# Performance work log

Hardware: AMD Instinct MI355X
Metric: run time of the kernel (lower is better)

Reference implementation:

```python
import jax, jax.numpy as jnp
import numpy as np

B, IN, H = 16384, 1024, 1024


def setup_inputs() -> dict:
    key = jax.random.key(0)
    ks = jax.random.split(key, 16)
    stdv = 1.0 / np.sqrt(H)
    u = lambda k, shape: jax.random.uniform(k, shape, jnp.float32, -stdv, stdv)
    return {
        "input": jax.random.normal(ks[0], (B, IN), jnp.float32),
        "prev_h": jax.random.normal(ks[1], (B, H), jnp.float32),
        "prev_c": jax.random.normal(ks[2], (B, H), jnp.float32),
        "weight_xi": u(ks[3], (IN, H)), "weight_hi": u(ks[4], (H, H)),
        "weight_xf": u(ks[5], (IN, H)), "weight_hf": u(ks[6], (H, H)),
        "weight_xu": u(ks[7], (IN, H)), "weight_hu": u(ks[8], (H, H)),
        "weight_xo": u(ks[9], (IN, H)), "weight_ho": u(ks[10], (H, H)),
        "bias_i": u(ks[11], (H,)), "bias_f": u(ks[12], (H,)),
        "bias_o": u(ks[13], (H,)), "bias_u": u(ks[14], (H,)),
    }


def reference(input, prev_h, prev_c,
              weight_xi, weight_hi, weight_xf, weight_hf,
              weight_xu, weight_hu, weight_xo, weight_ho,
              bias_i, bias_f, bias_o, bias_u):
    i = jax.nn.sigmoid(input @ weight_xi + prev_h @ weight_hi + bias_i)
    f = jax.nn.sigmoid(input @ weight_xf + prev_h @ weight_hf + bias_f)
    o = jax.nn.sigmoid(input @ weight_xo + prev_h @ weight_ho + bias_o)
    u = jnp.tanh(input @ weight_xu + prev_h @ weight_hu + bias_u)
    c = f * prev_c + i * u
    h = o * jnp.tanh(c)
    return (h, c)
```

## Files before the change

kernel.cpp:

```cpp
#include <hip/hip_runtime.h>
#include <hip/hip_bf16.h>
#include <stdint.h>


typedef short bf16x8 __attribute__((ext_vector_type(8)));
typedef unsigned short u16x8 __attribute__((ext_vector_type(8)));
typedef float f32x4 __attribute__((ext_vector_type(4)));

__device__ __forceinline__ unsigned short f2bf(float f) {
    union { float f; uint32_t u; } v; v.f = f;
    uint32_t r = v.u + 0x7FFFu + ((v.u >> 16) & 1u);
    return (unsigned short)(r >> 16);
}

__device__ __forceinline__ float fsig(float x) { return 1.0f / (1.0f + __expf(-x)); }
__device__ __forceinline__ float ftanh(float x) { return 2.0f * fsig(2.0f * x) - 1.0f; }

__global__ __launch_bounds__(256) void pack_a_kernel(const float* __restrict__ input,
                                                     const float* __restrict__ prev_h,
                                                     unsigned short* __restrict__ Apk) {
    long idx = (long)blockIdx.x * 256 + threadIdx.x;
    long e0 = idx * 8;
    int b = (int)(e0 >> 11);
    int k = (int)(e0 & 2047);
    const float* src = (k < 1024) ? (input + (size_t)b * 1024 + k)
                                  : (prev_h + (size_t)b * 1024 + (k - 1024));
    float4 lo = *(const float4*)src;
    float4 hi = *(const float4*)(src + 4);
    u16x8 o;
    o[0] = f2bf(lo.x); o[1] = f2bf(lo.y); o[2] = f2bf(lo.z); o[3] = f2bf(lo.w);
    o[4] = f2bf(hi.x); o[5] = f2bf(hi.y); o[6] = f2bf(hi.z); o[7] = f2bf(hi.w);
    *(u16x8*)(Apk + e0) = o;
}

__global__ __launch_bounds__(256) void pack_b_kernel(
        const float* __restrict__ wxi, const float* __restrict__ wxf,
        const float* __restrict__ wxo, const float* __restrict__ wxu,
        const float* __restrict__ whi, const float* __restrict__ whf,
        const float* __restrict__ who, const float* __restrict__ whu,
        unsigned short* __restrict__ Bpk) {
    int idx = blockIdx.x * 256 + threadIdx.x;
    int g  = idx >> 18;
    int r  = idx & 262143;
    int kc = r >> 10;
    int j  = r & 1023;
    const float* wx = (g == 0) ? wxi : (g == 1) ? wxf : (g == 2) ? wxo : wxu;
    const float* wh = (g == 0) ? whi : (g == 1) ? whf : (g == 2) ? who : whu;
    int k0 = kc * 8;
    const float* src = (k0 < 1024) ? (wx + (size_t)k0 * 1024 + j)
                                   : (wh + (size_t)(k0 - 1024) * 1024 + j);
    u16x8 o;
#pragma unroll
    for (int t = 0; t < 8; ++t) o[t] = f2bf(src[(size_t)t * 1024]);
    *(u16x8*)(Bpk + (((size_t)(g * 1024 + j)) << 11) + k0) = o;
}

__global__ __launch_bounds__(256, 2) void lstm_gemm_kernel(
        const unsigned short* __restrict__ Apk,
        const unsigned short* __restrict__ Bpk,
        const float* __restrict__ prev_c,
        const float* __restrict__ bi, const float* __restrict__ bf_,
        const float* __restrict__ bo, const float* __restrict__ bu,
        float* __restrict__ out_h, float* __restrict__ out_c) {
    __shared__ __align__(16) unsigned char smem[65536];
    const int tid = threadIdx.x;
    const int w = tid >> 6;
    const int l = tid & 63;
    const int bid = blockIdx.x;
    const int tileCol = bid & 15;
    const int tileRow = bid >> 4;
    const int rowBase = tileRow * 128;
    const int jBase = tileCol * 64;

    f32x4 acc[8][4];
    const f32x4 vzero = {0.f, 0.f, 0.f, 0.f};
#pragma unroll
    for (int m = 0; m < 8; ++m)
#pragma unroll
        for (int n = 0; n < 4; ++n) acc[m][n] = vzero;

    auto stage = [&](int buf, int kt) {
        unsigned short* As = (unsigned short*)(smem + buf * 24576);
        unsigned short* Bs = (unsigned short*)(smem + buf * 24576 + 8192);
        const int k0 = kt * 32;
#pragma unroll
        for (int s = 0; s < 2; ++s) {
            int ch = w + s * 4;
            int e0 = (ch * 64 + l) * 8;
            int rr = e0 >> 5, cc = e0 & 31;
            const unsigned short* gp = Apk + (size_t)(rowBase + rr) * 2048 + k0 + cc;
            __builtin_amdgcn_global_load_lds((__attribute__((address_space(1))) void*)gp,
                                             (__attribute__((address_space(3))) void*)(As + ch * 512),
                                             16, 0, 0);
        }
#pragma unroll
        for (int s = 0; s < 4; ++s) {
            int e0 = (s * 64 + l) * 8;
            int cc = e0 >> 5, kk = e0 & 31;
            const unsigned short* gp = Bpk + (((size_t)(w * 1024 + jBase + cc)) << 11) + k0 + kk;
            __builtin_amdgcn_global_load_lds((__attribute__((address_space(1))) void*)gp,
                                             (__attribute__((address_space(3))) void*)(Bs + w * 2048 + s * 512),
                                             16, 0, 0);
        }
    };

    int buf = 0;
    stage(0, 0);
    __syncthreads();

    const int lr = l & 15;
    const int lk = (l >> 4) * 8;

    for (int kt = 0; kt < 64; ++kt) {
        if (kt + 1 < 64) stage(buf ^ 1, kt + 1);
        const unsigned short* As = (const unsigned short*)(smem + buf * 24576);
        const unsigned short* Bs = (const unsigned short*)(smem + buf * 24576 + 8192) + w * 2048;
        bf16x8 af[8], bfr[4];
#pragma unroll
        for (int m = 0; m < 8; ++m) af[m] = *(const bf16x8*)(As + (m * 16 + lr) * 32 + lk);
#pragma unroll
        for (int n = 0; n < 4; ++n) bfr[n] = *(const bf16x8*)(Bs + (n * 16 + lr) * 32 + lk);
#pragma unroll
        for (int m = 0; m < 8; ++m)
#pragma unroll
            for (int n = 0; n < 4; ++n)
                acc[m][n] = __builtin_amdgcn_mfma_f32_16x16x32_bf16(af[m], bfr[n], acc[m][n], 0, 0, 0);
        __syncthreads();
        buf ^= 1;
    }

    float* ep = (float*)smem;
#pragma unroll
    for (int half = 0; half < 2; ++half) {
        if (half) __syncthreads();
#pragma unroll
        for (int m = 0; m < 4; ++m) {
#pragma unroll
            for (int n = 0; n < 4; ++n) {
                int col = n * 16 + lr;
                int row0 = m * 16 + (l >> 4) * 4;
#pragma unroll
                for (int t = 0; t < 4; ++t)
                    ep[(w * 64 + row0 + t) * 64 + col] = acc[half * 4 + m][n][t];
            }
        }
        __syncthreads();
        int r = tid >> 2;
        int c0 = (tid & 3) * 16;
        int grow = rowBase + half * 64 + r;
        int gcol = jBase + c0;
        const float* pc = prev_c + (size_t)grow * 1024 + gcol;
        float* ph = out_h + (size_t)grow * 1024 + gcol;
        float* pcc = out_c + (size_t)grow * 1024 + gcol;
#pragma unroll
        for (int q = 0; q < 4; ++q) {
            int c = c0 + q * 4;
            f32x4 pi = *(const f32x4*)(ep + 0 * 4096 + r * 64 + c);
            f32x4 pf = *(const f32x4*)(ep + 1 * 4096 + r * 64 + c);
            f32x4 po = *(const f32x4*)(ep + 2 * 4096 + r * 64 + c);
            f32x4 pu = *(const f32x4*)(ep + 3 * 4096 + r * 64 + c);
            f32x4 vbi = *(const f32x4*)(bi + gcol + q * 4);
            f32x4 vbf = *(const f32x4*)(bf_ + gcol + q * 4);
            f32x4 vbo = *(const f32x4*)(bo + gcol + q * 4);
            f32x4 vbu = *(const f32x4*)(bu + gcol + q * 4);
            f32x4 pcv = *(const f32x4*)(pc + q * 4);
            f32x4 hv, cv;
#pragma unroll
            for (int t = 0; t < 4; ++t) {
                float ii = fsig(pi[t] + vbi[t]);
                float ff = fsig(pf[t] + vbf[t]);
                float oo = fsig(po[t] + vbo[t]);
                float uu = ftanh(pu[t] + vbu[t]);
                float ccv = ff * pcv[t] + ii * uu;
                cv[t] = ccv;
                hv[t] = oo * ftanh(ccv);
            }
            *(f32x4*)(ph + q * 4) = hv;
            *(f32x4*)(pcc + q * 4) = cv;
        }
    }
}

extern "C" void kernel_launch(void* const* d_in, const int* in_sizes, int n_in,
                              void* d_out, int out_size, void* d_ws, size_t ws_size,
                              hipStream_t stream) {
    const float* input  = (const float*)d_in[0];
    const float* prev_h = (const float*)d_in[1];
    const float* prev_c = (const float*)d_in[2];
    const float* wxi = (const float*)d_in[3];
    const float* whi = (const float*)d_in[4];
    const float* wxf = (const float*)d_in[5];
    const float* whf = (const float*)d_in[6];
    const float* wxu = (const float*)d_in[7];
    const float* whu = (const float*)d_in[8];
    const float* wxo = (const float*)d_in[9];
    const float* who = (const float*)d_in[10];
    const float* bi  = (const float*)d_in[11];
    const float* bf_ = (const float*)d_in[12];
    const float* bo  = (const float*)d_in[13];
    const float* bu  = (const float*)d_in[14];

    unsigned short* Apk = (unsigned short*)d_ws;
    unsigned short* Bpk = (unsigned short*)((char*)d_ws + (size_t)67108864);

    float* out_h = (float*)d_out;
    float* out_c = out_h + (size_t)16384 * 1024;

    pack_a_kernel<<<dim3(16384), dim3(256), 0, stream>>>(input, prev_h, Apk);
    pack_b_kernel<<<dim3(4096), dim3(256), 0, stream>>>(wxi, wxf, wxo, wxu,
                                                        whi, whf, who, whu, Bpk);
    lstm_gemm_kernel<<<dim3(2048), dim3(256), 0, stream>>>(Apk, Bpk, prev_c,
                                                           bi, bf_, bo, bu, out_h, out_c);
}
```

Baseline: 400.8 us.

## Restructure LSTM GEMM into 4-stage pipelined 256x256 tiles with swizzled LDS

The fused GEMM now uses 512-thread blocks, each computing 256 rows by 64 columns across all four gates. Operands go through a 4-deep global_load_lds ring buffer with explicit vmcnt waits and split barriers, so loads for later k-tiles overlap the MFMAs of the current one. The kernel also adds an XOR swizzle on LDS to cut bank conflicts, raises MFMA wave priority with setprio, and remaps block IDs so neighbouring blocks share tiles in cache. The epilogue now applies the gate math straight from the accumulator registers instead of staging through LDS. In exchange it uses 128KB of LDS, which lowers occupancy, and the output stores are less coalesced.

```diff
diff --git a/kernel.cpp b/kernel.cpp
--- a/kernel.cpp
+++ b/kernel.cpp
@@ -1,6 +1,7 @@
 #include <hip/hip_runtime.h>
 #include <hip/hip_bf16.h>
 #include <stdint.h>
+#include <type_traits>
 
 
 typedef short bf16x8 __attribute__((ext_vector_type(8)));
@@ -55,130 +56,144 @@
     *(u16x8*)(Bpk + (((size_t)(g * 1024 + j)) << 11) + k0) = o;
 }
 
-__global__ __launch_bounds__(256, 2) void lstm_gemm_kernel(
+
+#define GLL(gp, lp) __builtin_amdgcn_global_load_lds( \
+        (__attribute__((address_space(1))) void*)(gp), \
+        (__attribute__((address_space(3))) void*)(lp), 16, 0, 0)
+
+#define BAR() do { asm volatile("" ::: "memory"); __builtin_amdgcn_s_barrier(); \
+                   asm volatile("" ::: "memory"); } while (0)
+
+__global__ __launch_bounds__(512, 2) void lstm_gemm_kernel(
         const unsigned short* __restrict__ Apk,
         const unsigned short* __restrict__ Bpk,
         const float* __restrict__ prev_c,
         const float* __restrict__ bi, const float* __restrict__ bf_,
         const float* __restrict__ bo, const float* __restrict__ bu,
         float* __restrict__ out_h, float* __restrict__ out_c) {
-    __shared__ __align__(16) unsigned char smem[65536];
+    __shared__ __align__(16) unsigned char smem[131072];
     const int tid = threadIdx.x;
-    const int w = tid >> 6;
-    const int l = tid & 63;
+    const int w = tid >> 6, l = tid & 63;
+    const int lr = l & 15, s4 = l >> 4;
+    const int wm = w >> 2, wq = w & 3;
+
     const int bid = blockIdx.x;
-    const int tileCol = bid & 15;
-    const int tileRow = bid >> 4;
-    const int rowBase = tileRow * 128;
+    const int sw = ((bid & 7) << 7) + (bid >> 3);
+    const int tileRow = sw & 63, tileCol = sw >> 6;
+    const int rowBase = tileRow * 256;
     const int jBase = tileCol * 64;
+
+    const int swr = ((s4 ^ ((lr >> 1) & 3)) << 4);
+
+    int aoff[8], boff[4];
+#pragma unroll
+    for (int m = 0; m < 8; ++m) aoff[m] = (wm * 128 + m * 16 + lr) * 64 + swr;
+#pragma unroll
+    for (int g = 0; g < 4; ++g) boff[g] = 16384 + (g * 64 + wq * 16 + lr) * 64 + swr;
+
+    const int slot = (l & 3) ^ ((l >> 3) & 3);
+    const int rloc = w * 16 + (l >> 2);
+    const unsigned short* aSrc0 = Apk + (size_t)(rowBase + rloc) * 2048 + slot * 8;
+    const unsigned short* aSrc1 = Apk + (size_t)(rowBase + 128 + rloc) * 2048 + slot * 8;
+    const int br0 = rloc, br1 = 128 + rloc;
+    const unsigned short* bSrc0 = Bpk + (((size_t)((br0 >> 6) * 1024 + jBase + (br0 & 63))) << 11) + slot * 8;
+    const unsigned short* bSrc1 = Bpk + (((size_t)((br1 >> 6) * 1024 + jBase + (br1 & 63))) << 11) + slot * 8;
+    const int aDst0 = w * 1024;
+    const int aDst1 = 8192 + w * 1024;
+    const int bDst0 = 16384 + w * 1024;
+    const int bDst1 = 24576 + w * 1024;
+
+#define STAGE_A(BUFB, T) do { \
+        GLL(aSrc0 + (size_t)(T) * 32, smem + (BUFB) + aDst0); \
+        GLL(aSrc1 + (size_t)(T) * 32, smem + (BUFB) + aDst1); } while (0)
+#define STAGE_B(BUFB, T) do { \
+        GLL(bSrc0 + (size_t)(T) * 32, smem + (BUFB) + bDst0); \
+        GLL(bSrc1 + (size_t)(T) * 32, smem + (BUFB) + bDst1); } while (0)
 
     f32x4 acc[8][4];
     const f32x4 vzero = {0.f, 0.f, 0.f, 0.f};
 #pragma unroll
     for (int m = 0; m < 8; ++m)
 #pragma unroll
-        for (int n = 0; n < 4; ++n) acc[m][n] = vzero;
-
-    auto stage = [&](int buf, int kt) {
-        unsigned short* As = (unsigned short*)(smem + buf * 24576);
-        unsigned short* Bs = (unsigned short*)(smem + buf * 24576 + 8192);
-        const int k0 = kt * 32;
-#pragma unroll
-        for (int s = 0; s < 2; ++s) {
-            int ch = w + s * 4;
-            int e0 = (ch * 64 + l) * 8;
-            int rr = e0 >> 5, cc = e0 & 31;
-            const unsigned short* gp = Apk + (size_t)(rowBase + rr) * 2048 + k0 + cc;
-            __builtin_amdgcn_global_load_lds((__attribute__((address_space(1))) void*)gp,
-                                             (__attribute__((address_space(3))) void*)(As + ch * 512),
-                                             16, 0, 0);
-        }
-#pragma unroll
-        for (int s = 0; s < 4; ++s) {
-            int e0 = (s * 64 + l) * 8;
-            int cc = e0 >> 5, kk = e0 & 31;
-            const unsigned short* gp = Bpk + (((size_t)(w * 1024 + jBase + cc)) << 11) + k0 + kk;
-            __builtin_amdgcn_global_load_lds((__attribute__((address_space(1))) void*)gp,
-                                             (__attribute__((address_space(3))) void*)(Bs + w * 2048 + s * 512),
-                                             16, 0, 0);
-        }
+        for (int g = 0; g < 4; ++g) acc[m][g] = vzero;
+
+    STAGE_A(0, 0);      STAGE_B(0, 0);
+    STAGE_A(32768, 1);  STAGE_B(32768, 1);
+    STAGE_A(65536, 2);  STAGE_B(65536, 2);
+    asm volatile("s_waitcnt vmcnt(8)" ::: "memory");
+    BAR();
+
+    auto ktile = [&](int t, auto vnc, auto stgc) {
+        constexpr int VN = decltype(vnc)::value;
+        constexpr bool STG = decltype(stgc)::value;
+        const int bt = (t & 3) * 32768;
+        const int b3 = ((t + 3) & 3) * 32768;
+        bf16x8 av[4], bv[4];
+#pragma unroll
+        for (int m = 0; m < 4; ++m) av[m] = *(const bf16x8*)(smem + bt + aoff[m]);
+#pragma unroll
+        for (int g = 0; g < 4; ++g) bv[g] = *(const bf16x8*)(smem + bt + boff[g]);
+        if constexpr (STG) STAGE_A(b3, t + 3);
+        BAR();
+        __builtin_amdgcn_s_setprio(1);
+#pragma unroll
+        for (int m = 0; m < 4; ++m)
+#pragma unroll
+            for (int g = 0; g < 4; ++g)
+                acc[m][g] = __builtin_amdgcn_mfma_f32_16x16x32_bf16(av[m], bv[g], acc[m][g], 0, 0, 0);
+        __builtin_amdgcn_s_setprio(0);
+        BAR();
+        bf16x8 av2[4];
+#pragma unroll
+        for (int m = 0; m < 4; ++m) av2[m] = *(const bf16x8*)(smem + bt + aoff[4 + m]);
+        if constexpr (STG) STAGE_B(b3, t + 3);
+        BAR();
+        __builtin_amdgcn_s_setprio(1);
+#pragma unroll
+        for (int m = 0; m < 4; ++m)
+#pragma unroll
+            for (int g = 0; g < 4; ++g)
+                acc[4 + m][g] = __builtin_amdgcn_mfma_f32_16x16x32_bf16(av2[m], bv[g], acc[4 + m][g], 0, 0, 0);
+        __builtin_amdgcn_s_setprio(0);
+        if constexpr (VN == 8) asm volatile("s_waitcnt vmcnt(8)" ::: "memory");
+        else if constexpr (VN == 4) asm volatile("s_waitcnt vmcnt(4)" ::: "memory");
+        else if constexpr (VN == 0) asm volatile("s_waitcnt vmcnt(0)" ::: "memory");
+        if constexpr (VN >= 0) BAR();
     };
 
-    int buf = 0;
-    stage(0, 0);
-    __syncthreads();
-
-    const int lr = l & 15;
-    const int lk = (l >> 4) * 8;
-
-    for (int kt = 0; kt < 64; ++kt) {
-        if (kt + 1 < 64) stage(buf ^ 1, kt + 1);
-        const unsigned short* As = (const unsigned short*)(smem + buf * 24576);
-        const unsigned short* Bs = (const unsigned short*)(smem + buf * 24576 + 8192) + w * 2048;
-        bf16x8 af[8], bfr[4];
-#pragma unroll
-        for (int m = 0; m < 8; ++m) af[m] = *(const bf16x8*)(As + (m * 16 + lr) * 32 + lk);
-#pragma unroll
-        for (int n = 0; n < 4; ++n) bfr[n] = *(const bf16x8*)(Bs + (n * 16 + lr) * 32 + lk);
-#pragma unroll
-        for (int m = 0; m < 8; ++m)
-#pragma unroll
-            for (int n = 0; n < 4; ++n)
-                acc[m][n] = __builtin_amdgcn_mfma_f32_16x16x32_bf16(af[m], bfr[n], acc[m][n], 0, 0, 0);
-        __syncthreads();
-        buf ^= 1;
-    }
-
-    float* ep = (float*)smem;
-#pragma unroll
-    for (int half = 0; half < 2; ++half) {
-        if (half) __syncthreads();
-#pragma unroll
-        for (int m = 0; m < 4; ++m) {
-#pragma unroll
-            for (int n = 0; n < 4; ++n) {
-                int col = n * 16 + lr;
-                int row0 = m * 16 + (l >> 4) * 4;
-#pragma unroll
-                for (int t = 0; t < 4; ++t)
-                    ep[(w * 64 + row0 + t) * 64 + col] = acc[half * 4 + m][n][t];
-            }
-        }
-        __syncthreads();
-        int r = tid >> 2;
-        int c0 = (tid & 3) * 16;
-        int grow = rowBase + half * 64 + r;
-        int gcol = jBase + c0;
-        const float* pc = prev_c + (size_t)grow * 1024 + gcol;
-        float* ph = out_h + (size_t)grow * 1024 + gcol;
-        float* pcc = out_c + (size_t)grow * 1024 + gcol;
-#pragma unroll
-        for (int q = 0; q < 4; ++q) {
-            int c = c0 + q * 4;
-            f32x4 pi = *(const f32x4*)(ep + 0 * 4096 + r * 64 + c);
-            f32x4 pf = *(const f32x4*)(ep + 1 * 4096 + r * 64 + c);
-            f32x4 po = *(const f32x4*)(ep + 2 * 4096 + r * 64 + c);
-            f32x4 pu = *(const f32x4*)(ep + 3 * 4096 + r * 64 + c);
-            f32x4 vbi = *(const f32x4*)(bi + gcol + q * 4);
-            f32x4 vbf = *(const f32x4*)(bf_ + gcol + q * 4);
-            f32x4 vbo = *(const f32x4*)(bo + gcol + q * 4);
-            f32x4 vbu = *(const f32x4*)(bu + gcol + q * 4);
-            f32x4 pcv = *(const f32x4*)(pc + q * 4);
-            f32x4 hv, cv;
-#pragma unroll
-            for (int t = 0; t < 4; ++t) {
-                float ii = fsig(pi[t] + vbi[t]);
-                float ff = fsig(pf[t] + vbf[t]);
-                float oo = fsig(po[t] + vbo[t]);
-                float uu = ftanh(pu[t] + vbu[t]);
-                float ccv = ff * pcv[t] + ii * uu;
-                cv[t] = ccv;
-                hv[t] = oo * ftanh(ccv);
-            }
-            *(f32x4*)(ph + q * 4) = hv;
-            *(f32x4*)(pcc + q * 4) = cv;
+    using ci8 = std::integral_constant<int, 8>;
+    using ci4 = std::integral_constant<int, 4>;
+    using ci0 = std::integral_constant<int, 0>;
+    using cim = std::integral_constant<int, -1>;
+    using bt_ = std::integral_constant<bool, true>;
+    using bf_c = std::integral_constant<bool, false>;
+
+#pragma unroll 1
+    for (int t = 0; t < 61; ++t) ktile(t, ci8{}, bt_{});
+    ktile(61, ci4{}, bf_c{});
+    ktile(62, ci0{}, bf_c{});
+    ktile(63, cim{}, bf_c{});
+
+    const int colIdx = jBase + wq * 16 + lr;
+    const float vbi = bi[colIdx], vbf = bf_[colIdx], vbo = bo[colIdx], vbu = bu[colIdx];
+    const int rowB = rowBase + wm * 128 + s4 * 4;
+#pragma unroll
+    for (int m = 0; m < 8; ++m) {
+#pragma unroll
+        for (int tt = 0; tt < 4; ++tt) {
+            const size_t idx = (size_t)(rowB + m * 16 + tt) * 1024 + colIdx;
+            float zi = acc[m][0][tt] + vbi;
+            float zf = acc[m][1][tt] + vbf;
+            float zo = acc[m][2][tt] + vbo;
+            float zu = acc[m][3][tt] + vbu;
+            float iv = fsig(zi), fv = fsig(zf), ov = fsig(zo), uv = ftanh(zu);
+            float cv = fv * prev_c[idx] + iv * uv;
+            out_c[idx] = cv;
+            out_h[idx] = ov * ftanh(cv);
         }
     }
+#undef STAGE_A
+#undef STAGE_B
 }
 
 extern "C" void kernel_launch(void* const* d_in, const int* in_sizes, int n_in,
@@ -209,6 +224,6 @@
     pack_a_kernel<<<dim3(16384), dim3(256), 0, stream>>>(input, prev_h, Apk);
     pack_b_kernel<<<dim3(4096), dim3(256), 0, stream>>>(wxi, wxf, wxo, wxu,
                                                         whi, whf, who, whu, Bpk);
-    lstm_gemm_kernel<<<dim3(2048), dim3(256), 0, stream>>>(Apk, Bpk, prev_c,
+    lstm_gemm_kernel<<<dim3(1024), dim3(512), 0, stream>>>(Apk, Bpk, prev_c,
                                                            bi, bf_, bo, bu, out_h, out_c);
 }
```

Result: faster. 351.2 us (-12.4%).
